# Performance work log

Measured on AMD Instinct MI355X. Metric: run time of the kernel, lower is better.

## Reference

```python
import jax, jax.numpy as jnp
import numpy as np

N_QUBITS = 6
DIM = 2 ** N_QUBITS  # 64
Q_LAYERS = 2
CHUNK = 16

# ---- single-qubit rotation gate matrices (batched over leading dim) ----

def _rx(t):
    c = jnp.cos(t / 2).astype(jnp.complex64)
    s = jnp.sin(t / 2).astype(jnp.complex64)
    return jnp.stack([jnp.stack([c, -1j * s], -1), jnp.stack([-1j * s, c], -1)], -2)

def _ry(t):
    c = jnp.cos(t / 2).astype(jnp.complex64)
    s = jnp.sin(t / 2).astype(jnp.complex64)
    return jnp.stack([jnp.stack([c, -s], -1), jnp.stack([s, c], -1)], -2)

def _rz(t):
    e = jnp.exp(-0.5j * t.astype(jnp.complex64))
    z = jnp.zeros_like(e)
    return jnp.stack([jnp.stack([e, z], -1), jnp.stack([z, jnp.conj(e)], -1)], -2)


def _apply_1q(state, gate, wire):
    # state: (B, 64) complex64; gate: (B,2,2). PennyLane wire 0 = most-significant bit.
    dl, dr = 2 ** wire, 2 ** (N_QUBITS - 1 - wire)
    s = state.reshape(-1, dl, 2, dr)
    s = jnp.einsum('bkj,bljr->blkr', gate, s)
    return s.reshape(-1, DIM)


def _apply_crx(state, theta, control, target):
    s = state.reshape((-1,) + (2,) * N_QUBITS)
    s = jnp.moveaxis(s, (control + 1, target + 1), (1, 2))
    g = _rx(theta)  # (B,2,2)
    s1 = jnp.einsum('bkj,bj...->bk...', g, s[:, 1])
    s = jnp.concatenate([s[:, :1], s1[:, None]], axis=1)
    s = jnp.moveaxis(s, (1, 2), (control + 1, target + 1))
    return s.reshape(-1, DIM)


def _ansatz(state, params, n_layers):
    # unified ansatz: per layer, RX/RY/RZ on each qubit, ring of CRX forward, ring of CRX backward
    idx = 0
    for _ in range(n_layers):
        for i in range(N_QUBITS):
            state = _apply_1q(state, _rx(params[:, idx]), i)
            state = _apply_1q(state, _ry(params[:, idx + 1]), i)
            state = _apply_1q(state, _rz(params[:, idx + 2]), i)
            idx += 3
        for i in range(N_QUBITS):
            state = _apply_crx(state, params[:, idx], i, (i + 1) % N_QUBITS)
            idx += 1
        for i in range(N_QUBITS - 1, -1, -1):
            state = _apply_crx(state, params[:, idx], i, (i - 1) % N_QUBITS)
            idx += 1
    return state


_PX = jnp.array([[0, 1], [1, 0]], jnp.complex64)
_PY = jnp.array([[0, -1j], [1j, 0]], jnp.complex64)
_PZ = jnp.array([[1, 0], [0, -1]], jnp.complex64)


def _expvals(state):
    # expectations of X_i, Y_i, Z_i for all qubits -> (B, 3*n_qubits)
    outs = []
    B = state.shape[0]
    for P in (_PX, _PY, _PZ):
        g = jnp.broadcast_to(P, (B, 2, 2))
        for i in range(N_QUBITS):
            ps = _apply_1q(state, g, i)
            outs.append(jnp.sum(jnp.conj(state) * ps, axis=1).real)
    return jnp.stack(outs, axis=1).astype(jnp.float32)


def _forward(x, emb_w, emb_b, att_w1, att_b1, att_w2, att_b2, proj_w, proj_b,
             mix_re, mix_im, qff_params, out_w, out_b, ln_g, ln_b,
             cls_w1, cls_b1, cls_w2, cls_b2):
    B, C, T = x.shape
    # classical feature extractor: (B,C,T) -> (B,T,D)
    feats = jnp.einsum('bct,cd->btd', x, emb_w) + emb_b
    D = feats.shape[-1]
    n_chunks = T // CHUNK
    xc = feats.reshape(B, n_chunks, CHUNK, D)
    # attention-weighted chunk aggregation
    h = jnp.tanh(xc @ att_w1 + att_b1)
    scores = h @ att_w2 + att_b2                      # (B,nc,CHUNK,1)
    w = jax.nn.softmax(scores, axis=2)
    chunks = jnp.sum(w * xc, axis=2)                  # (B,nc,D)
    # quantum attention core: per-chunk ansatz params
    params = jax.nn.sigmoid(chunks @ proj_w + proj_b)  # (B,nc,60)
    flat = params.reshape(B * n_chunks, -1)
    state0 = jnp.zeros((B * n_chunks, DIM), jnp.complex64).at[:, 0].set(1.0)
    evolved = _ansatz(state0, flat, Q_LAYERS).reshape(B, n_chunks, DIM)
    # LCU mixing
    coeffs = (mix_re + 1j * mix_im).astype(jnp.complex64)
    coeffs = coeffs / (jnp.abs(coeffs).sum() + 1e-8)
    mixed = jnp.einsum('bti,t->bi', evolved, coeffs)
    norms = jnp.linalg.norm(mixed, axis=1, keepdims=True)
    mixed = mixed / (norms + 1e-9)
    # quantum feed-forward (shared params) + multi-observable measurement
    qp = jnp.broadcast_to(qff_params, (B, qff_params.shape[0]))
    qstate = _ansatz(mixed, qp, 1)
    qfeat = _expvals(qstate)                          # (B,18)
    out = qfeat @ out_w + out_b                       # (B,D)
    # LayerNorm
    mu = out.mean(-1, keepdims=True)
    var = out.var(-1, keepdims=True)
    out = (out - mu) / jnp.sqrt(var + 1e-5) * ln_g + ln_b
    # classifier head
    h2 = jax.nn.relu(out @ cls_w1 + cls_b1)
    return h2 @ cls_w2 + cls_b2


def setup_inputs() -> dict:
    key = jax.random.key(0)
    ks = jax.random.split(key, 20)
    B, C, T, D = 128, 64, 2048, 256
    NC = T // CHUNK        # 128 chunks
    NCP = 5 * N_QUBITS * Q_LAYERS  # 60 circuit params
    def nrm(k, shape, scale=0.05):
        return jax.random.normal(k, shape, jnp.float32) * scale
    return {
        'x': jax.random.normal(ks[0], (B, C, T), jnp.float32),
        'emb_w': nrm(ks[1], (C, D)), 'emb_b': nrm(ks[2], (D,)),
        'att_w1': nrm(ks[3], (D, D // 2)), 'att_b1': nrm(ks[4], (D // 2,)),
        'att_w2': nrm(ks[5], (D // 2, 1)), 'att_b2': nrm(ks[6], (1,)),
        'proj_w': nrm(ks[7], (D, NCP)), 'proj_b': nrm(ks[8], (NCP,)),
        'mix_re': jax.random.uniform(ks[9], (NC,), jnp.float32),
        'mix_im': jax.random.uniform(ks[10], (NC,), jnp.float32),
        'qff_params': nrm(ks[11], (5 * N_QUBITS,), 0.1),
        'out_w': nrm(ks[12], (3 * N_QUBITS, D)), 'out_b': nrm(ks[13], (D,)),
        'ln_g': jnp.ones((D,), jnp.float32), 'ln_b': jnp.zeros((D,), jnp.float32),
        'cls_w1': nrm(ks[14], (D, D)), 'cls_b1': nrm(ks[15], (D,)),
        'cls_w2': nrm(ks[16], (D, 2)), 'cls_b2': nrm(ks[17], (2,)),
    }


def reference(x, emb_w, emb_b, att_w1, att_b1, att_w2, att_b2, proj_w, proj_b,
              mix_re, mix_im, qff_params, out_w, out_b, ln_g, ln_b,
              cls_w1, cls_b1, cls_w2, cls_b2):
    return _forward(x, emb_w, emb_b, att_w1, att_b1, att_w2, att_b2, proj_w, proj_b,
                    mix_re, mix_im, qff_params, out_w, out_b, ln_g, ln_b,
                    cls_w1, cls_b1, cls_w2, cls_b2)
```

## Files before the change

kernel.cpp:

```cpp
#include <hip/hip_runtime.h>
#include <math.h>

#define NQ    6
#define QDIM  64
#define BB    128
#define CC    64
#define TT    2048
#define DD    256
#define NCH   128
#define CHLEN 16
#define HH    128
#define NCP   60

typedef __bf16 bf16x8 __attribute__((ext_vector_type(8)));
typedef float  f32x4  __attribute__((ext_vector_type(4)));

__device__ __forceinline__ float fast_tanh(float x) {
  float e = __expf(2.f * x);
  return 1.f - 2.f / (e + 1.f);
}

__device__ __forceinline__ float wave_sum(float v) {
#pragma unroll
  for (int off = 32; off >= 1; off >>= 1) v += __shfl_xor(v, off, 64);
  return v;
}

__device__ __forceinline__ void g_rx(float& re, float& im, int lane, int m, float half) {
  float c = __cosf(half), s = __sinf(half);
  float pre = __shfl_xor(re, m, 64);
  float pim = __shfl_xor(im, m, 64);
  float nre = c * re + s * pim;
  float nim = c * im - s * pre;
  re = nre; im = nim;
}
__device__ __forceinline__ void g_ry(float& re, float& im, int lane, int m, float half) {
  float c = __cosf(half), s = __sinf(half);
  float pre = __shfl_xor(re, m, 64);
  float pim = __shfl_xor(im, m, 64);
  float sg = (lane & m) ? s : -s;
  re = c * re + sg * pre;
  im = c * im + sg * pim;
}
__device__ __forceinline__ void g_rz(float& re, float& im, int lane, int m, float half) {
  float c = __cosf(half), s = __sinf(half);
  float sg = (lane & m) ? s : -s;
  float nre = c * re - sg * im;
  float nim = c * im + sg * re;
  re = nre; im = nim;
}
__device__ __forceinline__ void g_crx(float& re, float& im, int lane, int mc, int mt, float half) {
  float c = __cosf(half), s = __sinf(half);
  float pre = __shfl_xor(re, mt, 64);
  float pim = __shfl_xor(im, mt, 64);
  if (lane & mc) {
    float nre = c * re + s * pim;
    float nim = c * im - s * pre;
    re = nre; im = nim;
  }
}
__device__ __forceinline__ void ansatz_layer(float& re, float& im, int lane,
                                             const float* p) {
#pragma unroll
  for (int q = 0; q < 6; ++q) {
    int m = 1 << (5 - q);
    g_rx(re, im, lane, m, 0.5f * p[3 * q + 0]);
    g_ry(re, im, lane, m, 0.5f * p[3 * q + 1]);
    g_rz(re, im, lane, m, 0.5f * p[3 * q + 2]);
  }
#pragma unroll
  for (int q = 0; q < 6; ++q)
    g_crx(re, im, lane, 1 << (5 - q), 1 << (5 - ((q + 1) % 6)), 0.5f * p[18 + q]);
#pragma unroll
  for (int q = 5; q >= 0; --q)
    g_crx(re, im, lane, 1 << (5 - q), 1 << (5 - ((q + 5) % 6)), 0.5f * p[24 + (5 - q)]);
}

__global__ __launch_bounds__(256) void k0_prep(
    const float* __restrict__ emb_w, const float* __restrict__ emb_b,
    const float* __restrict__ att_w1, const float* __restrict__ att_b1,
    const float* __restrict__ proj_w, const float* __restrict__ proj_b,
    __bf16* __restrict__ WfH, __bf16* __restrict__ WfL,
    __bf16* __restrict__ PfH, __bf16* __restrict__ PfL,
    float* __restrict__ b_fused, float* __restrict__ pb_fused) {
  int idx = blockIdx.x * 256 + threadIdx.x;
  if (idx < 8192) {
    int j = idx & 127, k = idx >> 7;
    float a = 0.f;
    for (int d = 0; d < 256; ++d)
      a = fmaf(emb_w[k * 256 + d], att_w1[d * 128 + j], a);
    __bf16 h = (__bf16)a;
    WfH[j * 64 + k] = h; WfL[j * 64 + k] = (__bf16)(a - (float)h);
  } else if (idx < 12288) {
    int i = idx - 8192;
    int n = i & 63, k = i >> 6;
    float a = 0.f;
    if (n < 60)
      for (int d = 0; d < 256; ++d)
        a = fmaf(emb_w[k * 256 + d], proj_w[d * 60 + n], a);
    __bf16 h = (__bf16)a;
    PfH[n * 64 + k] = h; PfL[n * 64 + k] = (__bf16)(a - (float)h);
  } else if (idx < 12416) {
    int j = idx - 12288;
    float a = att_b1[j];
    for (int d = 0; d < 256; ++d) a = fmaf(emb_b[d], att_w1[d * 128 + j], a);
    b_fused[j] = a;
  } else if (idx < 12480) {
    int n = idx - 12416;
    float a = 0.f;
    if (n < 60) {
      a = proj_b[n];
      for (int d = 0; d < 256; ++d) a = fmaf(emb_b[d], proj_w[d * 60 + n], a);
    }
    pb_fused[n] = a;
  }
}

__global__ __launch_bounds__(256) void k1_fused(
    const float* __restrict__ x, const float* __restrict__ att_w2,
    const __bf16* __restrict__ WfH, const __bf16* __restrict__ WfL,
    const __bf16* __restrict__ PfH, const __bf16* __restrict__ PfL,
    const float* __restrict__ b_fused, const float* __restrict__ pb_fused,
    float2* __restrict__ evolved) {
  const int blk = blockIdx.x;
  const int b = blk >> 6, cp = blk & 63;
  const int tid = threadIdx.x, wv = tid >> 6, lane = tid & 63;
  const int l15 = lane & 15, quad = lane >> 4;

  __shared__ float xtile[32][68];
  __shared__ float scoreS[4][32];
  __shared__ float wSm[2][16];
  __shared__ float xaggS[2][64];
  __shared__ float paramsS[2][60];

  {
#pragma unroll
    for (int pass = 0; pass < 2; ++pass) {
      int k = pass * 32 + (tid >> 3), t4 = tid & 7;
      float4 v = *(const float4*)(x + ((size_t)(b * 64 + k)) * 2048 + cp * 32 + t4 * 4);
      xtile[t4 * 4 + 0][k] = v.x; xtile[t4 * 4 + 1][k] = v.y;
      xtile[t4 * 4 + 2][k] = v.z; xtile[t4 * 4 + 3][k] = v.w;
    }
  }
  __syncthreads();

  f32x4 acc[2][2];
#pragma unroll
  for (int mt = 0; mt < 2; ++mt)
#pragma unroll
    for (int jt = 0; jt < 2; ++jt) acc[mt][jt] = (f32x4){0.f, 0.f, 0.f, 0.f};
#pragma unroll
  for (int mt = 0; mt < 2; ++mt) {
    bf16x8 ah[2], al[2];
#pragma unroll
    for (int ks = 0; ks < 2; ++ks) {
      const float* src = &xtile[mt * 16 + l15][ks * 32 + 8 * quad];
      float4 u0 = *(const float4*)src, u1 = *(const float4*)(src + 4);
      float vals[8] = {u0.x, u0.y, u0.z, u0.w, u1.x, u1.y, u1.z, u1.w};
#pragma unroll
      for (int j = 0; j < 8; ++j) {
        __bf16 h = (__bf16)vals[j];
        ah[ks][j] = h;
        al[ks][j] = (__bf16)(vals[j] - (float)h);
      }
    }
#pragma unroll
    for (int jt = 0; jt < 2; ++jt)
#pragma unroll
      for (int ks = 0; ks < 2; ++ks) {
        const size_t row = (size_t)(wv * 32 + jt * 16 + l15) * 64 + ks * 32 + 8 * quad;
        bf16x8 bh = *(const bf16x8*)(WfH + row);
        bf16x8 bl = *(const bf16x8*)(WfL + row);
        acc[mt][jt] = __builtin_amdgcn_mfma_f32_16x16x32_bf16(ah[ks], bh, acc[mt][jt], 0, 0, 0);
        acc[mt][jt] = __builtin_amdgcn_mfma_f32_16x16x32_bf16(al[ks], bh, acc[mt][jt], 0, 0, 0);
        acc[mt][jt] = __builtin_amdgcn_mfma_f32_16x16x32_bf16(ah[ks], bl, acc[mt][jt], 0, 0, 0);
      }
  }
  {
    float w2v[2], b1v[2];
#pragma unroll
    for (int jt = 0; jt < 2; ++jt) {
      int j = wv * 32 + jt * 16 + l15;
      w2v[jt] = att_w2[j];
      b1v[jt] = b_fused[j];
    }
#pragma unroll
    for (int mt = 0; mt < 2; ++mt)
#pragma unroll
      for (int r = 0; r < 4; ++r) {
        float sc = fast_tanh(acc[mt][0][r] + b1v[0]) * w2v[0] +
                   fast_tanh(acc[mt][1][r] + b1v[1]) * w2v[1];
        sc += __shfl_xor(sc, 1, 64);
        sc += __shfl_xor(sc, 2, 64);
        sc += __shfl_xor(sc, 4, 64);
        sc += __shfl_xor(sc, 8, 64);
        if (l15 == 0) scoreS[wv][mt * 16 + quad * 4 + r] = sc;
      }
  }
  __syncthreads();

  if (tid < 2) {
    float s[16], mx = -1e30f;
#pragma unroll
    for (int t = 0; t < 16; ++t) {
      int tt = tid * 16 + t;
      s[t] = (scoreS[0][tt] + scoreS[1][tt]) + (scoreS[2][tt] + scoreS[3][tt]);
      mx = fmaxf(mx, s[t]);
    }
    float sum = 0.f;
#pragma unroll
    for (int t = 0; t < 16; ++t) { s[t] = __expf(s[t] - mx); sum += s[t]; }
    float inv = 1.f / sum;
#pragma unroll
    for (int t = 0; t < 16; ++t) wSm[tid][t] = s[t] * inv;
  }
  __syncthreads();

  if (tid < 128) {
    const int c = tid >> 6, k = tid & 63;
    float a = 0.f;
#pragma unroll
    for (int t = 0; t < 16; ++t) a = fmaf(wSm[c][t], xtile[c * 16 + t][k], a);
    xaggS[c][k] = a;
  }
  __syncthreads();

  {
    const int jout = wv * 16 + l15;
    f32x4 acc3 = (f32x4){0.f, 0.f, 0.f, 0.f};
#pragma unroll
    for (int ks = 0; ks < 2; ++ks) {
      const size_t row = (size_t)jout * 64 + ks * 32 + 8 * quad;
      bf16x8 bh = *(const bf16x8*)(PfH + row);
      bf16x8 bl = *(const bf16x8*)(PfL + row);
      bf16x8 ax = (bf16x8)(__bf16)0.f, alx = (bf16x8)(__bf16)0.f;
      if (l15 < 2) {
        const float* cs = &xaggS[l15][ks * 32 + 8 * quad];
        float4 u0 = *(const float4*)cs, u1 = *(const float4*)(cs + 4);
        float vals[8] = {u0.x, u0.y, u0.z, u0.w, u1.x, u1.y, u1.z, u1.w};
#pragma unroll
        for (int j = 0; j < 8; ++j) {
          __bf16 h = (__bf16)vals[j];
          ax[j] = h;
          alx[j] = (__bf16)(vals[j] - (float)h);
        }
      }
      acc3 = __builtin_amdgcn_mfma_f32_16x16x32_bf16(ax, bh, acc3, 0, 0, 0);
      acc3 = __builtin_amdgcn_mfma_f32_16x16x32_bf16(alx, bh, acc3, 0, 0, 0);
      acc3 = __builtin_amdgcn_mfma_f32_16x16x32_bf16(ax, bl, acc3, 0, 0, 0);
    }
    if (jout < 60 && quad == 0) {
      float pbias = pb_fused[jout];
#pragma unroll
      for (int r = 0; r < 2; ++r) {
        float a = acc3[r] + pbias;
        paramsS[r][jout] = 1.f / (1.f + __expf(-a));
      }
    }
  }
  __syncthreads();

  if (wv < 2) {
    float re = (lane == 0) ? 1.f : 0.f, im = 0.f;
    const float* p = paramsS[wv];
    ansatz_layer(re, im, lane, p);
    ansatz_layer(re, im, lane, p + 30);
    evolved[((size_t)b * NCH + cp * 2 + wv) * QDIM + lane] = make_float2(re, im);
  }
}

__global__ __launch_bounds__(512) void k3_head(
    const float2* __restrict__ evolved, const float* __restrict__ mix_re,
    const float* __restrict__ mix_im, const float* __restrict__ qff,
    const float* __restrict__ out_w, const float* __restrict__ out_b,
    const float* __restrict__ ln_g, const float* __restrict__ ln_b,
    const float* __restrict__ cls_w1, const float* __restrict__ cls_b1,
    const float* __restrict__ cls_w2, const float* __restrict__ cls_b2,
    float* __restrict__ outp) {
  const int b = blockIdx.x, tid = threadIdx.x, wv = tid >> 6, lane = tid & 63;
  __shared__ float mreS[8][64], mimS[8][64];
  __shared__ float qfeatS[18];
  __shared__ float outS[DD];
  __shared__ float redS[8];
  __shared__ float clsR[2][DD];

  float are = 0.f, aim = 0.f;
#pragma unroll 4
  for (int t = wv * 16; t < wv * 16 + 16; ++t) {
    float2 e = evolved[((size_t)b * NCH + t) * QDIM + lane];
    float cr = mix_re[t], ci = mix_im[t];
    are = fmaf(cr, e.x, are); are = fmaf(-ci, e.y, are);
    aim = fmaf(cr, e.y, aim); aim = fmaf(ci, e.x, aim);
  }
  mreS[wv][lane] = are; mimS[wv][lane] = aim;
  __syncthreads();

  if (wv == 0) {
    float r0 = mix_re[lane], i0 = mix_im[lane];
    float r1 = mix_re[lane + 64], i1 = mix_im[lane + 64];
    float sp = sqrtf(r0 * r0 + i0 * i0) + sqrtf(r1 * r1 + i1 * i1);
    float S = wave_sum(sp) + 1e-8f;
    float re = 0.f, im = 0.f;
#pragma unroll
    for (int w = 0; w < 8; ++w) { re += mreS[w][lane]; im += mimS[w][lane]; }
    float invS = 1.f / S;
    re *= invS; im *= invS;
    float n2 = wave_sum(re * re + im * im);
    float scl = 1.f / (sqrtf(n2) + 1e-9f);
    re *= scl; im *= scl;
    float qp[30];
#pragma unroll
    for (int i = 0; i < 30; ++i) qp[i] = qff[i];
    ansatz_layer(re, im, lane, qp);
#pragma unroll
    for (int q = 0; q < 6; ++q) {
      int m = 1 << (5 - q);
      float pre = __shfl_xor(re, m, 64), pim = __shfl_xor(im, m, 64);
      float vx = re * pre + im * pim;
      float vy = (lane & m) ? (im * pre - re * pim) : (re * pim - im * pre);
      float vz = (lane & m) ? -(re * re + im * im) : (re * re + im * im);
      vx = wave_sum(vx); vy = wave_sum(vy); vz = wave_sum(vz);
      if (lane == 0) { qfeatS[q] = vx; qfeatS[6 + q] = vy; qfeatS[12 + q] = vz; }
    }
  }
  __syncthreads();

  float o = 0.f, dv = 0.f;
  if (tid < 256) {
    o = out_b[tid];
#pragma unroll
    for (int k = 0; k < 18; ++k) o = fmaf(qfeatS[k], out_w[k * DD + tid], o);
    float s1 = wave_sum(o);
    if (lane == 0) redS[wv] = s1;
  }
  __syncthreads();
  float mu = (redS[0] + redS[1] + redS[2] + redS[3]) * (1.f / 256.f);
  if (tid < 256) {
    dv = o - mu;
    float s2 = wave_sum(dv * dv);
    if (lane == 0) redS[wv] = s2;
  }
  __syncthreads();
  float var = (redS[0] + redS[1] + redS[2] + redS[3]) * (1.f / 256.f);
  if (tid < 256) {
    outS[tid] = dv / sqrtf(var + 1e-5f) * ln_g[tid] + ln_b[tid];
  }
  __syncthreads();

  {
    const int dd = tid & 255, hh = tid >> 8;
    float r = (hh == 0) ? cls_b1[dd] : 0.f;
#pragma unroll 8
    for (int d = hh * 128; d < hh * 128 + 128; ++d)
      r = fmaf(outS[d], cls_w1[(size_t)d * DD + dd], r);
    clsR[hh][dd] = r;
  }
  __syncthreads();
  if (tid < 256) {
    float r = fmaxf(clsR[0][tid] + clsR[1][tid], 0.f);
    float p0 = wave_sum(r * cls_w2[tid * 2 + 0]);
    float p1 = wave_sum(r * cls_w2[tid * 2 + 1]);
    if (lane == 0) { mreS[0][wv] = p0; mreS[1][wv] = p1; }
  }
  __syncthreads();
  if (tid == 0) {
    outp[b * 2 + 0] = (mreS[0][0] + mreS[0][1]) + (mreS[0][2] + mreS[0][3]) + cls_b2[0];
    outp[b * 2 + 1] = (mreS[1][0] + mreS[1][1]) + (mreS[1][2] + mreS[1][3]) + cls_b2[1];
  }
}

extern "C" void kernel_launch(void* const* d_in, const int* in_sizes, int n_in,
                              void* d_out, int out_size, void* d_ws, size_t ws_size,
                              hipStream_t stream) {
  const float* x      = (const float*)d_in[0];
  const float* emb_w  = (const float*)d_in[1];
  const float* emb_b  = (const float*)d_in[2];
  const float* att_w1 = (const float*)d_in[3];
  const float* att_b1 = (const float*)d_in[4];
  const float* att_w2 = (const float*)d_in[5];
  const float* proj_w = (const float*)d_in[7];
  const float* proj_b = (const float*)d_in[8];
  const float* mix_re = (const float*)d_in[9];
  const float* mix_im = (const float*)d_in[10];
  const float* qff    = (const float*)d_in[11];
  const float* out_w  = (const float*)d_in[12];
  const float* out_b  = (const float*)d_in[13];
  const float* ln_g   = (const float*)d_in[14];
  const float* ln_b   = (const float*)d_in[15];
  const float* cls_w1 = (const float*)d_in[16];
  const float* cls_b1 = (const float*)d_in[17];
  const float* cls_w2 = (const float*)d_in[18];
  const float* cls_b2 = (const float*)d_in[19];

  char* ws = (char*)d_ws;
  float2* evolved = (float2*)ws;
  size_t off = 8388608;
  __bf16* WfH = (__bf16*)(ws + off); off += 16384;
  __bf16* WfL = (__bf16*)(ws + off); off += 16384;
  __bf16* PfH = (__bf16*)(ws + off); off += 8192;
  __bf16* PfL = (__bf16*)(ws + off); off += 8192;
  float* b_fused  = (float*)(ws + off); off += 512;
  float* pb_fused = (float*)(ws + off); off += 256;

  k0_prep<<<49, 256, 0, stream>>>(emb_w, emb_b, att_w1, att_b1, proj_w, proj_b,
                                  WfH, WfL, PfH, PfL, b_fused, pb_fused);
  k1_fused<<<BB * 64, 256, 0, stream>>>(
      x, att_w2, WfH, WfL, PfH, PfL, b_fused, pb_fused, evolved);
  k3_head<<<BB, 512, 0, stream>>>(evolved, mix_re, mix_im, qff, out_w, out_b,
                                  ln_g, ln_b, cls_w1, cls_b1, cls_w2, cls_b2,
                                  (float*)d_out);
}
```

Measured before the change: 214.6 us.

## Fuse complex mixing into chunk kernel via atomics and double chunks per block

Each chunk block now handles four chunks instead of two, reusing the loaded weight fragments across more MFMA tiles, and runs all four waves through the ansatz. Instead of writing the full evolved state buffer to global memory, each wave multiplies its state by the complex mixing coefficient and atomically accumulates into a small per-batch buffer zeroed in the prep kernel. The head kernel reads that buffer directly, folds the 1/S normalisation into the norm epsilon, and spreads the Pauli expectation reductions across six waves. This removes an 8 MB intermediate write and read, at the cost of float atomics contention (32 blocks per batch row) and nondeterministic summation order.

Result: no change. 217.7 us (+1.4%).

```diff
diff --git a/kernel.cpp b/kernel.cpp
--- a/kernel.cpp
+++ b/kernel.cpp
@@ -82,7 +82,8 @@
     const float* __restrict__ proj_w, const float* __restrict__ proj_b,
     __bf16* __restrict__ WfH, __bf16* __restrict__ WfL,
     __bf16* __restrict__ PfH, __bf16* __restrict__ PfL,
-    float* __restrict__ b_fused, float* __restrict__ pb_fused) {
+    float* __restrict__ b_fused, float* __restrict__ pb_fused,
+    float* __restrict__ mixedRaw) {
   int idx = blockIdx.x * 256 + threadIdx.x;
   if (idx < 8192) {
     int j = idx & 127, k = idx >> 7;
@@ -113,79 +114,90 @@
       for (int d = 0; d < 256; ++d) a = fmaf(emb_b[d], proj_w[d * 60 + n], a);
     }
     pb_fused[n] = a;
-  }
-}
-
-__global__ __launch_bounds__(256) void k1_fused(
+  } else if (idx >= 16384) {
+    mixedRaw[idx - 16384] = 0.f;
+  }
+}
+
+__global__ __launch_bounds__(256, 4) void k1_fused(
     const float* __restrict__ x, const float* __restrict__ att_w2,
     const __bf16* __restrict__ WfH, const __bf16* __restrict__ WfL,
     const __bf16* __restrict__ PfH, const __bf16* __restrict__ PfL,
     const float* __restrict__ b_fused, const float* __restrict__ pb_fused,
-    float2* __restrict__ evolved) {
+    const float* __restrict__ mix_re, const float* __restrict__ mix_im,
+    float* __restrict__ mixedRaw) {
   const int blk = blockIdx.x;
-  const int b = blk >> 6, cp = blk & 63;
+  const int b = blk >> 5, cq = blk & 31;
   const int tid = threadIdx.x, wv = tid >> 6, lane = tid & 63;
   const int l15 = lane & 15, quad = lane >> 4;
 
-  __shared__ float xtile[32][68];
-  __shared__ float scoreS[4][32];
-  __shared__ float wSm[2][16];
-  __shared__ float xaggS[2][64];
-  __shared__ float paramsS[2][60];
-
-  {
-#pragma unroll
-    for (int pass = 0; pass < 2; ++pass) {
-      int k = pass * 32 + (tid >> 3), t4 = tid & 7;
-      float4 v = *(const float4*)(x + ((size_t)(b * 64 + k)) * 2048 + cp * 32 + t4 * 4);
+  __shared__ float xtile[64][68];
+  __shared__ float scoreS[4][64];
+  __shared__ float wSm[4][16];
+  __shared__ float xaggS[4][64];
+  __shared__ float paramsS[4][60];
+
+  {
+#pragma unroll
+    for (int pass = 0; pass < 4; ++pass) {
+      int k = pass * 16 + (tid >> 4), t4 = tid & 15;
+      float4 v = *(const float4*)(x + ((size_t)(b * 64 + k)) * 2048 + cq * 64 + t4 * 4);
       xtile[t4 * 4 + 0][k] = v.x; xtile[t4 * 4 + 1][k] = v.y;
       xtile[t4 * 4 + 2][k] = v.z; xtile[t4 * 4 + 3][k] = v.w;
     }
   }
-  __syncthreads();
-
-  f32x4 acc[2][2];
-#pragma unroll
-  for (int mt = 0; mt < 2; ++mt)
+  float w2v[2], b1v[2];
+#pragma unroll
+  for (int jt = 0; jt < 2; ++jt) {
+    int j = wv * 32 + jt * 16 + l15;
+    w2v[jt] = att_w2[j];
+    b1v[jt] = b_fused[j];
+  }
+  __syncthreads();
+
+  f32x4 acc[4][2];
+#pragma unroll
+  for (int mt = 0; mt < 4; ++mt)
 #pragma unroll
     for (int jt = 0; jt < 2; ++jt) acc[mt][jt] = (f32x4){0.f, 0.f, 0.f, 0.f};
-#pragma unroll
-  for (int mt = 0; mt < 2; ++mt) {
-    bf16x8 ah[2], al[2];
-#pragma unroll
-    for (int ks = 0; ks < 2; ++ks) {
-      const float* src = &xtile[mt * 16 + l15][ks * 32 + 8 * quad];
-      float4 u0 = *(const float4*)src, u1 = *(const float4*)(src + 4);
-      float vals[8] = {u0.x, u0.y, u0.z, u0.w, u1.x, u1.y, u1.z, u1.w};
-#pragma unroll
-      for (int j = 0; j < 8; ++j) {
-        __bf16 h = (__bf16)vals[j];
-        ah[ks][j] = h;
-        al[ks][j] = (__bf16)(vals[j] - (float)h);
-      }
-    }
+  {
+    bf16x8 bh[2][2], bl[2][2];
 #pragma unroll
     for (int jt = 0; jt < 2; ++jt)
 #pragma unroll
       for (int ks = 0; ks < 2; ++ks) {
         const size_t row = (size_t)(wv * 32 + jt * 16 + l15) * 64 + ks * 32 + 8 * quad;
-        bf16x8 bh = *(const bf16x8*)(WfH + row);
-        bf16x8 bl = *(const bf16x8*)(WfL + row);
-        acc[mt][jt] = __builtin_amdgcn_mfma_f32_16x16x32_bf16(ah[ks], bh, acc[mt][jt], 0, 0, 0);
-        acc[mt][jt] = __builtin_amdgcn_mfma_f32_16x16x32_bf16(al[ks], bh, acc[mt][jt], 0, 0, 0);
-        acc[mt][jt] = __builtin_amdgcn_mfma_f32_16x16x32_bf16(ah[ks], bl, acc[mt][jt], 0, 0, 0);
+        bh[jt][ks] = *(const bf16x8*)(WfH + row);
+        bl[jt][ks] = *(const bf16x8*)(WfL + row);
       }
-  }
-  {
-    float w2v[2], b1v[2];
-#pragma unroll
-    for (int jt = 0; jt < 2; ++jt) {
-      int j = wv * 32 + jt * 16 + l15;
-      w2v[jt] = att_w2[j];
-      b1v[jt] = b_fused[j];
-    }
-#pragma unroll
-    for (int mt = 0; mt < 2; ++mt)
+#pragma unroll
+    for (int mt = 0; mt < 4; ++mt) {
+      bf16x8 ah[2], al[2];
+#pragma unroll
+      for (int ks = 0; ks < 2; ++ks) {
+        const float* src = &xtile[mt * 16 + l15][ks * 32 + 8 * quad];
+        float4 u0 = *(const float4*)src, u1 = *(const float4*)(src + 4);
+        float vals[8] = {u0.x, u0.y, u0.z, u0.w, u1.x, u1.y, u1.z, u1.w};
+#pragma unroll
+        for (int j = 0; j < 8; ++j) {
+          __bf16 h = (__bf16)vals[j];
+          ah[ks][j] = h;
+          al[ks][j] = (__bf16)(vals[j] - (float)h);
+        }
+      }
+#pragma unroll
+      for (int jt = 0; jt < 2; ++jt)
+#pragma unroll
+        for (int ks = 0; ks < 2; ++ks) {
+          acc[mt][jt] = __builtin_amdgcn_mfma_f32_16x16x32_bf16(ah[ks], bh[jt][ks], acc[mt][jt], 0, 0, 0);
+          acc[mt][jt] = __builtin_amdgcn_mfma_f32_16x16x32_bf16(al[ks], bh[jt][ks], acc[mt][jt], 0, 0, 0);
+          acc[mt][jt] = __builtin_amdgcn_mfma_f32_16x16x32_bf16(ah[ks], bl[jt][ks], acc[mt][jt], 0, 0, 0);
+        }
+    }
+  }
+  {
+#pragma unroll
+    for (int mt = 0; mt < 4; ++mt)
 #pragma unroll
       for (int r = 0; r < 4; ++r) {
         float sc = fast_tanh(acc[mt][0][r] + b1v[0]) * w2v[0] +
@@ -199,7 +211,7 @@
   }
   __syncthreads();
 
-  if (tid < 2) {
+  if (tid < 4) {
     float s[16], mx = -1e30f;
 #pragma unroll
     for (int t = 0; t < 16; ++t) {
@@ -216,7 +228,7 @@
   }
   __syncthreads();
 
-  if (tid < 128) {
+  {
     const int c = tid >> 6, k = tid & 63;
     float a = 0.f;
 #pragma unroll
@@ -234,7 +246,7 @@
       bf16x8 bh = *(const bf16x8*)(PfH + row);
       bf16x8 bl = *(const bf16x8*)(PfL + row);
       bf16x8 ax = (bf16x8)(__bf16)0.f, alx = (bf16x8)(__bf16)0.f;
-      if (l15 < 2) {
+      if (l15 < 4) {
         const float* cs = &xaggS[l15][ks * 32 + 8 * quad];
         float4 u0 = *(const float4*)cs, u1 = *(const float4*)(cs + 4);
         float vals[8] = {u0.x, u0.y, u0.z, u0.w, u1.x, u1.y, u1.z, u1.w};
@@ -252,7 +264,7 @@
     if (jout < 60 && quad == 0) {
       float pbias = pb_fused[jout];
 #pragma unroll
-      for (int r = 0; r < 2; ++r) {
+      for (int r = 0; r < 4; ++r) {
         float a = acc3[r] + pbias;
         paramsS[r][jout] = 1.f / (1.f + __expf(-a));
       }
@@ -260,17 +272,23 @@
   }
   __syncthreads();
 
-  if (wv < 2) {
+  {
     float re = (lane == 0) ? 1.f : 0.f, im = 0.f;
     const float* p = paramsS[wv];
     ansatz_layer(re, im, lane, p);
     ansatz_layer(re, im, lane, p + 30);
-    evolved[((size_t)b * NCH + cp * 2 + wv) * QDIM + lane] = make_float2(re, im);
+    const int t = cq * 4 + wv;
+    float cr = mix_re[t], ci = mix_im[t];
+    float wr = cr * re - ci * im;
+    float wi = cr * im + ci * re;
+    float* mp = mixedRaw + (((size_t)b * 64 + lane) << 1);
+    atomicAdd(mp + 0, wr);
+    atomicAdd(mp + 1, wi);
   }
 }
 
 __global__ __launch_bounds__(512) void k3_head(
-    const float2* __restrict__ evolved, const float* __restrict__ mix_re,
+    const float* __restrict__ mixedRaw, const float* __restrict__ mix_re,
     const float* __restrict__ mix_im, const float* __restrict__ qff,
     const float* __restrict__ out_w, const float* __restrict__ out_b,
     const float* __restrict__ ln_g, const float* __restrict__ ln_b,
@@ -278,50 +296,39 @@
     const float* __restrict__ cls_w2, const float* __restrict__ cls_b2,
     float* __restrict__ outp) {
   const int b = blockIdx.x, tid = threadIdx.x, wv = tid >> 6, lane = tid & 63;
-  __shared__ float mreS[8][64], mimS[8][64];
+  __shared__ float stateS[2][64];
   __shared__ float qfeatS[18];
   __shared__ float outS[DD];
   __shared__ float redS[8];
   __shared__ float clsR[2][DD];
 
-  float are = 0.f, aim = 0.f;
-#pragma unroll 4
-  for (int t = wv * 16; t < wv * 16 + 16; ++t) {
-    float2 e = evolved[((size_t)b * NCH + t) * QDIM + lane];
-    float cr = mix_re[t], ci = mix_im[t];
-    are = fmaf(cr, e.x, are); are = fmaf(-ci, e.y, are);
-    aim = fmaf(cr, e.y, aim); aim = fmaf(ci, e.x, aim);
-  }
-  mreS[wv][lane] = are; mimS[wv][lane] = aim;
-  __syncthreads();
-
   if (wv == 0) {
+    float2 m = ((const float2*)mixedRaw)[b * 64 + lane];
     float r0 = mix_re[lane], i0 = mix_im[lane];
     float r1 = mix_re[lane + 64], i1 = mix_im[lane + 64];
     float sp = sqrtf(r0 * r0 + i0 * i0) + sqrtf(r1 * r1 + i1 * i1);
     float S = wave_sum(sp) + 1e-8f;
-    float re = 0.f, im = 0.f;
-#pragma unroll
-    for (int w = 0; w < 8; ++w) { re += mreS[w][lane]; im += mimS[w][lane]; }
-    float invS = 1.f / S;
-    re *= invS; im *= invS;
+    float re = m.x, im = m.y;
     float n2 = wave_sum(re * re + im * im);
-    float scl = 1.f / (sqrtf(n2) + 1e-9f);
+    float scl = 1.f / (sqrtf(n2) + S * 1e-9f);
     re *= scl; im *= scl;
     float qp[30];
 #pragma unroll
     for (int i = 0; i < 30; ++i) qp[i] = qff[i];
     ansatz_layer(re, im, lane, qp);
-#pragma unroll
-    for (int q = 0; q < 6; ++q) {
-      int m = 1 << (5 - q);
-      float pre = __shfl_xor(re, m, 64), pim = __shfl_xor(im, m, 64);
-      float vx = re * pre + im * pim;
-      float vy = (lane & m) ? (im * pre - re * pim) : (re * pim - im * pre);
-      float vz = (lane & m) ? -(re * re + im * im) : (re * re + im * im);
-      vx = wave_sum(vx); vy = wave_sum(vy); vz = wave_sum(vz);
-      if (lane == 0) { qfeatS[q] = vx; qfeatS[6 + q] = vy; qfeatS[12 + q] = vz; }
-    }
+    stateS[0][lane] = re; stateS[1][lane] = im;
+  }
+  __syncthreads();
+
+  if (wv < 6) {
+    const int m = 1 << (5 - wv);
+    float re = stateS[0][lane], im = stateS[1][lane];
+    float pre = stateS[0][lane ^ m], pim = stateS[1][lane ^ m];
+    float vx = re * pre + im * pim;
+    float vy = (lane & m) ? (im * pre - re * pim) : (re * pim - im * pre);
+    float vz = (lane & m) ? -(re * re + im * im) : (re * re + im * im);
+    vx = wave_sum(vx); vy = wave_sum(vy); vz = wave_sum(vz);
+    if (lane == 0) { qfeatS[wv] = vx; qfeatS[6 + wv] = vy; qfeatS[12 + wv] = vz; }
   }
   __syncthreads();
 
@@ -360,12 +367,12 @@
     float r = fmaxf(clsR[0][tid] + clsR[1][tid], 0.f);
     float p0 = wave_sum(r * cls_w2[tid * 2 + 0]);
     float p1 = wave_sum(r * cls_w2[tid * 2 + 1]);
-    if (lane == 0) { mreS[0][wv] = p0; mreS[1][wv] = p1; }
+    if (lane == 0) { stateS[0][wv] = p0; stateS[1][wv] = p1; }
   }
   __syncthreads();
   if (tid == 0) {
-    outp[b * 2 + 0] = (mreS[0][0] + mreS[0][1]) + (mreS[0][2] + mreS[0][3]) + cls_b2[0];
-    outp[b * 2 + 1] = (mreS[1][0] + mreS[1][1]) + (mreS[1][2] + mreS[1][3]) + cls_b2[1];
+    outp[b * 2 + 0] = (stateS[0][0] + stateS[0][1]) + (stateS[0][2] + stateS[0][3]) + cls_b2[0];
+    outp[b * 2 + 1] = (stateS[1][0] + stateS[1][1]) + (stateS[1][2] + stateS[1][3]) + cls_b2[1];
   }
 }
 
@@ -393,8 +400,8 @@
   const float* cls_b2 = (const float*)d_in[19];
 
   char* ws = (char*)d_ws;
-  float2* evolved = (float2*)ws;
-  size_t off = 8388608;
+  float* mixedRaw = (float*)ws;
+  size_t off = 65536;
   __bf16* WfH = (__bf16*)(ws + off); off += 16384;
   __bf16* WfL = (__bf16*)(ws + off); off += 16384;
   __bf16* PfH = (__bf16*)(ws + off); off += 8192;
@@ -402,11 +409,13 @@
   float* b_fused  = (float*)(ws + off); off += 512;
   float* pb_fused = (float*)(ws + off); off += 256;
 
-  k0_prep<<<49, 256, 0, stream>>>(emb_w, emb_b, att_w1, att_b1, proj_w, proj_b,
-                                  WfH, WfL, PfH, PfL, b_fused, pb_fused);
-  k1_fused<<<BB * 64, 256, 0, stream>>>(
-      x, att_w2, WfH, WfL, PfH, PfL, b_fused, pb_fused, evolved);
-  k3_head<<<BB, 512, 0, stream>>>(evolved, mix_re, mix_im, qff, out_w, out_b,
+  k0_prep<<<128, 256, 0, stream>>>(emb_w, emb_b, att_w1, att_b1, proj_w, proj_b,
+                                   WfH, WfL, PfH, PfL, b_fused, pb_fused,
+                                   mixedRaw);
+  k1_fused<<<BB * 32, 256, 0, stream>>>(
+      x, att_w2, WfH, WfL, PfH, PfL, b_fused, pb_fused, mix_re, mix_im,
+      mixedRaw);
+  k3_head<<<BB, 512, 0, stream>>>(mixedRaw, mix_re, mix_im, qff, out_w, out_b,
                                   ln_g, ln_b, cls_w1, cls_b1, cls_w2, cls_b2,
                                   (float*)d_out);
 }
```
